# Kernel tuning notes

Hardware: AMD Instinct MI355X
Metric: run time of the kernel (lower is better)

Reference implementation:

```python
import jax, jax.numpy as jnp
import numpy as np

# Protocol constants (config.protocol); standard DCE-MRI values.
TR = 0.005                       # repetition time [s]
ALPHA = 15.0 / 180.0 * np.pi     # flip angle [rad]
DELTT = 4.0 / 60.0               # temporal resolution [min]
R1_RELAX = 4.5                   # contrast agent relaxivity [/mM/s]
N_TIME = 112
BATCH = 262144


def setup_inputs() -> dict:
    key = jax.random.key(0)
    k1, k2, k3, k4, k5 = jax.random.split(key, 5)
    # Physiologically plausible positive ranges (avoid division blowups).
    ktrans = jax.random.uniform(k1, (BATCH, 1), jnp.float32, 0.01, 1.0)
    vp = jax.random.uniform(k2, (BATCH, 1), jnp.float32, 0.0, 0.1)
    ve = jax.random.uniform(k3, (BATCH, 1), jnp.float32, 0.05, 1.0)
    T10 = jax.random.uniform(k4, (BATCH, 1), jnp.float32, 0.5, 2.0)
    CAp = jax.random.uniform(k5, (BATCH, N_TIME), jnp.float32, 0.0, 1.0)
    return {"ktrans": ktrans, "vp": vp, "ve": ve, "T10": T10, "CAp": CAp}


def _cae(CAp, ktrans, ve):
    # Original: Toeplitz matrix ce_x with ce[b,i] = ktrans*deltt *
    #   sum_{j<=i} CAp[b,j] * exp(-ktrans/ve * (i-j) * deltt)
    # == first-order IIR recurrence c_i = decay * c_{i-1} + CAp[:, i].
    decay = jnp.exp(-ktrans / ve * DELTT)[:, 0]  # [B]

    def step(c, cap_t):
        c = c * decay + cap_t
        return c, c

    c0 = jnp.zeros(CAp.shape[0], CAp.dtype)
    _, cs = jax.lax.scan(step, c0, CAp.T)  # cs: [N, B]
    return (ktrans * DELTT) * cs.T          # [B, N]


def reference(ktrans, vp, ve, T10, CAp):
    ce = _cae(CAp, ktrans, ve)                 # [B, N]
    ct = vp * CAp + ce                         # tissue concentration
    R1t = 1.0 / T10 + R1_RELAX * ct            # [B, N]
    e = jnp.exp(-TR * R1t)
    s = (1.0 - e) * np.sin(ALPHA) / (1.0 - e * np.cos(ALPHA))
    return s * 20.0


if __name__ == "__main__":
    out = reference(**setup_inputs())
    print(out.shape, out.dtype)
```

## Files before the change

### kernel.cpp

```cpp
#include <hip/hip_runtime.h>

#define N_TIME  112
#define BATCH   262144
#define NF4ROW  28
#define NCH     7

__device__ __forceinline__ float sig(float cap, float c, float vp,
                                     float kd, float invT10) {
    const float TR     = 0.005f;
    const float R1     = 4.5f;
    const float SINA20 = 20.0f * 0.25881904510252074f;
    const float COSA   = 0.96592582628906829f;
    float ct = vp * cap + kd * c;
    float e  = __expf(-TR * (invT10 + R1 * ct));
    return (1.0f - e) * SINA20 * __builtin_amdgcn_rcpf(1.0f - e * COSA);
}

__global__ __launch_bounds__(256) void etofts_kernel(
    const float* __restrict__ ktrans_p,
    const float* __restrict__ vp_p,
    const float* __restrict__ ve_p,
    const float* __restrict__ T10_p,
    const float* __restrict__ cap_p,
    float* __restrict__ out_p)
{
    const int tid = blockIdx.x * blockDim.x + threadIdx.x;
    const int row = tid >> 2;
    const int t   = tid & 3;

    const float DELTT  = 4.0f / 60.0f;
    const float ktrans = ktrans_p[row];
    const float vp     = vp_p[row];
    const float ve     = ve_p[row];
    const float invT10 = __builtin_amdgcn_rcpf(T10_p[row]);
    const float kd     = ktrans * DELTT;

    const float d1  = __expf(-ktrans / ve * DELTT);
    const float d2  = d1 * d1;
    const float d3  = d2 * d1;
    const float d4  = d2 * d2;
    const float d8  = d4 * d4;
    const float d12 = d8 * d4;
    const float d16 = d8 * d8;
    const float dt4 = (t == 0) ? 1.0f : (t == 1) ? d4 : (t == 2) ? d8 : d12;

    const float4* capv = reinterpret_cast<const float4*>(cap_p) + (size_t)row * NF4ROW + t;
    float4*       outv = reinterpret_cast<float4*>(out_p)       + (size_t)row * NF4ROW + t;

    float4 x[NCH];
    #pragma unroll
    for (int ch = 0; ch < NCH; ++ch) x[ch] = capv[ch * 4];

    float s1[NCH], s2[NCH], s3[NCH], E[NCH], T[NCH];
    #pragma unroll
    for (int ch = 0; ch < NCH; ++ch) {
        float a0 = x[ch].x;
        float a1 = fmaf(d1, a0, x[ch].y);
        float a2 = fmaf(d1, a1, x[ch].z);
        float a3 = fmaf(d1, a2, x[ch].w);
        s1[ch] = a1; s2[ch] = a2; s3[ch] = a3;

        float S  = a3;
        float v1 = __shfl_up(S, 1, 4);
        if (t >= 1) S = fmaf(d4, v1, S);
        float v2 = __shfl_up(S, 2, 4);
        if (t >= 2) S = fmaf(d8, v2, S);

        E[ch] = __shfl_up(S, 1, 4);
        T[ch] = __shfl(S, 3, 4);
    }

    float C[NCH];
    C[0] = 0.0f;
    #pragma unroll
    for (int ch = 0; ch < NCH - 1; ++ch) C[ch + 1] = fmaf(d16, C[ch], T[ch]);

    #pragma unroll
    for (int ch = 0; ch < NCH; ++ch) {
        float tin = (t == 0) ? dt4 * C[ch] : fmaf(dt4, C[ch], E[ch]);

        float c0 = fmaf(d1, tin, x[ch].x);
        float c1 = fmaf(d2, tin, s1[ch]);
        float c2 = fmaf(d3, tin, s2[ch]);
        float c3 = fmaf(d4, tin, s3[ch]);

        float4 y;
        y.x = sig(x[ch].x, c0, vp, kd, invT10);
        y.y = sig(x[ch].y, c1, vp, kd, invT10);
        y.z = sig(x[ch].z, c2, vp, kd, invT10);
        y.w = sig(x[ch].w, c3, vp, kd, invT10);
        outv[ch * 4] = y;
    }
}

extern "C" void kernel_launch(void* const* d_in, const int* in_sizes, int n_in,
                              void* d_out, int out_size, void* d_ws, size_t ws_size,
                              hipStream_t stream) {
    const float* ktrans = (const float*)d_in[0];
    const float* vp     = (const float*)d_in[1];
    const float* ve     = (const float*)d_in[2];
    const float* T10    = (const float*)d_in[3];
    const float* CAp    = (const float*)d_in[4];
    float* out = (float*)d_out;

    dim3 block(256);
    dim3 grid((BATCH * 4) / 256);
    etofts_kernel<<<grid, block, 0, stream>>>(ktrans, vp, ve, T10, CAp, out);
}
```

Baseline: 43.88 us.

## Stage CAp and output through per-wave LDS tiles for contiguous global access

Each wavefront now loads its 16 rows of CAp as fully contiguous float4s into a padded LDS tile, then reads its strided per-thread chunks from LDS. Results are written back to the same LDS slots and stored to global memory contiguously. The goal is to replace the strided (stride-4 float4) global loads and stores with coalesced ones. This costs LDS traffic and 29-float4 row padding to avoid bank conflicts, and relies on wave-local ordering with no barrier between writing and reading the tile.

```diff
diff --git a/kernel.cpp b/kernel.cpp
--- a/kernel.cpp
+++ b/kernel.cpp
@@ -4,6 +4,8 @@
 #define BATCH   262144
 #define NF4ROW  28
 #define NCH     7
+#define RPW     16
+#define LP      29
 
 __device__ __forceinline__ float sig(float cap, float c, float vp,
                                      float kd, float invT10) {
@@ -24,15 +26,35 @@
     const float* __restrict__ cap_p,
     float* __restrict__ out_p)
 {
-    const int tid = blockIdx.x * blockDim.x + threadIdx.x;
-    const int row = tid >> 2;
-    const int t   = tid & 3;
+    __shared__ float4 tile[4][RPW * LP];
+
+    const int w    = threadIdx.x >> 6;
+    const int lane = threadIdx.x & 63;
+    const int g0   = blockIdx.x * 64 + w * RPW;
+
+    float4* wt = tile[w];
+
+    const float4* src = reinterpret_cast<const float4*>(cap_p) + (size_t)g0 * NF4ROW;
+    float4*       dst = reinterpret_cast<float4*>(out_p)       + (size_t)g0 * NF4ROW;
+
+    float4 ld[NCH];
+    int    slot[NCH];
+    #pragma unroll
+    for (int k = 0; k < NCH; ++k) {
+        int f   = lane + (k << 6);
+        ld[k]   = src[f];
+        slot[k] = (f / NF4ROW) * LP + (f % NF4ROW);
+    }
+
+    const int r    = lane >> 2;
+    const int t    = lane & 3;
+    const int grow = g0 + r;
 
     const float DELTT  = 4.0f / 60.0f;
-    const float ktrans = ktrans_p[row];
-    const float vp     = vp_p[row];
-    const float ve     = ve_p[row];
-    const float invT10 = __builtin_amdgcn_rcpf(T10_p[row]);
+    const float ktrans = ktrans_p[grow];
+    const float vp     = vp_p[grow];
+    const float ve     = ve_p[grow];
+    const float invT10 = __builtin_amdgcn_rcpf(T10_p[grow]);
     const float kd     = ktrans * DELTT;
 
     const float d1  = __expf(-ktrans / ve * DELTT);
@@ -44,12 +66,12 @@
     const float d16 = d8 * d8;
     const float dt4 = (t == 0) ? 1.0f : (t == 1) ? d4 : (t == 2) ? d8 : d12;
 
-    const float4* capv = reinterpret_cast<const float4*>(cap_p) + (size_t)row * NF4ROW + t;
-    float4*       outv = reinterpret_cast<float4*>(out_p)       + (size_t)row * NF4ROW + t;
+    #pragma unroll
+    for (int k = 0; k < NCH; ++k) wt[slot[k]] = ld[k];
 
     float4 x[NCH];
     #pragma unroll
-    for (int ch = 0; ch < NCH; ++ch) x[ch] = capv[ch * 4];
+    for (int ch = 0; ch < NCH; ++ch) x[ch] = wt[r * LP + ch * 4 + t];
 
     float s1[NCH], s2[NCH], s3[NCH], E[NCH], T[NCH];
     #pragma unroll
@@ -89,8 +111,11 @@
         y.y = sig(x[ch].y, c1, vp, kd, invT10);
         y.z = sig(x[ch].z, c2, vp, kd, invT10);
         y.w = sig(x[ch].w, c3, vp, kd, invT10);
-        outv[ch * 4] = y;
+        wt[r * LP + ch * 4 + t] = y;
     }
+
+    #pragma unroll
+    for (int k = 0; k < NCH; ++k) dst[lane + (k << 6)] = wt[slot[k]];
 }
 
 extern "C" void kernel_launch(void* const* d_in, const int* in_sizes, int n_in,
@@ -104,6 +129,6 @@
     float* out = (float*)d_out;
 
     dim3 block(256);
-    dim3 grid((BATCH * 4) / 256);
+    dim3 grid(BATCH / 64);
     etofts_kernel<<<grid, block, 0, stream>>>(ktrans, vp, ve, T10, CAp, out);
 }
```

After: 40.80 us. 7.0% less time.
